# Kernel optimization log

Measured on AMD Instinct MI355X. Metric: run time of the kernel, lower is better.

The kernel has to match this reference:

```python
import jax, jax.numpy as jnp
import numpy as np

N_ATOMS = 100_000
N_EDGES = 6_400_000
N_MOL = 128
Z_MAX = 90
KE = 14.3996
CUTOFF = 5.0


def setup_inputs() -> dict:
    key = jax.random.key(0)
    ks = jax.random.split(key, 9)
    partial_charges = jax.random.normal(ks[0], (N_ATOMS,), dtype=jnp.float32)
    Z = jax.random.randint(ks[1], (N_ATOMS,), 0, Z_MAX, dtype=jnp.int32)
    # Born exponents typically ~6-12
    ns = jax.random.uniform(ks[2], (N_ATOMS,), dtype=jnp.float32) * 4.0 + 6.0
    idx_m = jnp.sort(jax.random.randint(ks[3], (N_ATOMS,), 0, N_MOL, dtype=jnp.int32))
    idx_m = idx_m.at[-1].set(N_MOL - 1)
    # displacement vectors with norms bounded away from 0 to keep 1/d^n finite in fp32
    dirs = jax.random.normal(ks[4], (N_EDGES, 3), dtype=jnp.float32)
    dirs = dirs / jnp.linalg.norm(dirs, axis=1, keepdims=True)
    lengths = jax.random.uniform(ks[5], (N_EDGES, 1), dtype=jnp.float32) * 4.5 + 1.0
    Rij = dirs * lengths
    idx_i = jax.random.randint(ks[6], (N_EDGES,), 0, N_ATOMS, dtype=jnp.int32)
    idx_j = jax.random.randint(ks[7], (N_EDGES,), 0, N_ATOMS, dtype=jnp.int32)
    is_film = jax.random.randint(ks[8], (N_ATOMS,), 0, 2, dtype=jnp.int32)
    # dense realization of r0_dict: keyed by (is_film_i, is_film_j, Z_i, Z_j)
    r0_table = jax.random.uniform(jax.random.fold_in(key, 99), (2, 2, Z_MAX, Z_MAX), dtype=jnp.float32) * 1.5 + 0.5
    return {
        "partial_charges": partial_charges, "Z": Z, "ns": ns, "idx_m": idx_m,
        "Rij": Rij, "idx_i": idx_i, "idx_j": idx_j, "is_film": is_film,
        "r0_table": r0_table,
    }


def reference(partial_charges, Z, ns, idx_m, Rij, idx_i, idx_j, is_film, r0_table):
    q = partial_charges
    q_ij = jnp.abs(q[idx_i] * q[idx_j])                      # [E]
    d_ij = jnp.linalg.norm(Rij, axis=1)                      # [E]
    n_ij = ns[idx_i] + ns[idx_j] / 2.0                       # [E]
    r0_ij = r0_table[is_film[idx_i], is_film[idx_j], Z[idx_i], Z[idx_j]]  # [E]
    B_ij = q_ij * r0_ij ** (n_ij - 1.0) / n_ij               # [E]
    # shifted Born potential: B * (1/d^n - 1/cutoff^n)
    potential = B_ij * (d_ij ** (-n_ij) - CUTOFF ** (-n_ij))
    potential = jnp.where(d_ij <= CUTOFF, potential, jnp.zeros_like(potential))
    y = jax.ops.segment_sum(potential, idx_i, num_segments=N_ATOMS)  # edge -> atom
    y = jax.ops.segment_sum(y, idx_m, num_segments=N_MOL)            # atom -> molecule
    return 0.5 * KE * y
```

## Files before the change

kernel.cpp:

```cpp
#include <hip/hip_runtime.h>

#define NMOL 128
#define ZMAX 90
#define BLOCK 256

__device__ __forceinline__ float fast_exp2(float x) {
#if __has_builtin(__builtin_amdgcn_exp2f)
    return __builtin_amdgcn_exp2f(x);
#else
    return exp2f(x);
#endif
}
__device__ __forceinline__ float fast_log2(float x) {
#if __has_builtin(__builtin_amdgcn_logf)
    return __builtin_amdgcn_logf(x);
#else
    return log2f(x);
#endif
}
__device__ __forceinline__ float fast_rcp(float x) {
#if __has_builtin(__builtin_amdgcn_rcpf)
    return __builtin_amdgcn_rcpf(x);
#else
    return 1.0f / x;
#endif
}

__global__ void pack_atoms_kernel(const float* __restrict__ q,
                                  const int* __restrict__ Z,
                                  const float* __restrict__ ns,
                                  const int* __restrict__ idx_m,
                                  const int* __restrict__ is_film,
                                  float4* __restrict__ atoms,
                                  float* __restrict__ out, int nA) {
    int t = blockIdx.x * BLOCK + threadIdx.x;
    if (blockIdx.x == 0 && threadIdx.x < NMOL) out[threadIdx.x] = 0.0f;
    if (t < nA) {
        float4 a;
        a.x = q[t];
        a.y = ns[t];
        a.z = __int_as_float(Z[t] | (is_film[t] << 16));
        a.w = __int_as_float(idx_m[t]);
        atoms[t] = a;
    }
}

__device__ __forceinline__ float edge_pot(const float4* __restrict__ atoms,
                                          const float* __restrict__ r0_table,
                                          int i, int j,
                                          float x, float y, float z,
                                          int& mol) {
    constexpr float LOG2_CUT = 2.321928094887362f;
    const float4 ai = atoms[i];
    const float4 aj = atoms[j];
    const float d2 = fmaf(x, x, fmaf(y, y, z * z));

    int zi = __float_as_int(ai.z);
    int zj = __float_as_int(aj.z);
    const int fi = zi >> 16, fj = zj >> 16;
    zi &= 0xFFFF; zj &= 0xFFFF;
    const float r0 = r0_table[((fi * 2 + fj) * ZMAX + zi) * ZMAX + zj];

    const float qij = fabsf(ai.x * aj.x);
    const float n = fmaf(0.5f, aj.y, ai.y);
    const float B = qij * fast_exp2((n - 1.0f) * fast_log2(r0)) * fast_rcp(n);
    const float dpow = fast_exp2(-0.5f * n * fast_log2(d2));
    const float cpow = fast_exp2(-n * LOG2_CUT);

    mol = __float_as_int(ai.w);
    return (d2 <= 25.0f) ? B * (dpow - cpow) : 0.0f;
}

__global__ void __launch_bounds__(BLOCK)
edge_kernel(const float4* __restrict__ atoms,
            const float* __restrict__ r0_table,
            const float4* __restrict__ Rij4,
            const int4* __restrict__ idx_i4,
            const int4* __restrict__ idx_j4,
            float* __restrict__ out, int nE) {
    constexpr float HALF_KE = 7.1998f;

    __shared__ float bins[NMOL];
    for (int t = threadIdx.x; t < NMOL; t += BLOCK) bins[t] = 0.0f;
    __syncthreads();

    const int nE4 = nE >> 2;
    const int stride = gridDim.x * BLOCK;
    for (int t = blockIdx.x * BLOCK + threadIdx.x; t < nE4; t += stride) {
        const int4 ii = idx_i4[t];
        const int4 jj = idx_j4[t];
        const float4 ra = Rij4[3 * t + 0];
        const float4 rb = Rij4[3 * t + 1];
        const float4 rc = Rij4[3 * t + 2];

        int m0, m1, m2, m3;
        const float p0 = edge_pot(atoms, r0_table, ii.x, jj.x, ra.x, ra.y, ra.z, m0);
        const float p1 = edge_pot(atoms, r0_table, ii.y, jj.y, ra.w, rb.x, rb.y, m1);
        const float p2 = edge_pot(atoms, r0_table, ii.z, jj.z, rb.z, rb.w, rc.x, m2);
        const float p3 = edge_pot(atoms, r0_table, ii.w, jj.w, rc.y, rc.z, rc.w, m3);

        if (p0 != 0.0f) atomicAdd(&bins[m0], p0);
        if (p1 != 0.0f) atomicAdd(&bins[m1], p1);
        if (p2 != 0.0f) atomicAdd(&bins[m2], p2);
        if (p3 != 0.0f) atomicAdd(&bins[m3], p3);
    }

    const int tail_start = nE4 << 2;
    const int* idx_i = (const int*)idx_i4;
    const int* idx_j = (const int*)idx_j4;
    const float* Rij = (const float*)Rij4;
    for (int e = tail_start + blockIdx.x * BLOCK + threadIdx.x; e < nE; e += stride) {
        int m;
        const float p = edge_pot(atoms, r0_table, idx_i[e], idx_j[e],
                                 Rij[3 * e + 0], Rij[3 * e + 1], Rij[3 * e + 2], m);
        if (p != 0.0f) atomicAdd(&bins[m], p);
    }

    __syncthreads();
    for (int t = threadIdx.x; t < NMOL; t += BLOCK) {
        const float v = bins[t];
        if (v != 0.0f) atomicAdd(&out[t], v * HALF_KE);
    }
}

__global__ void __launch_bounds__(BLOCK)
edge_kernel_raw(const float* __restrict__ q,
                const int* __restrict__ Z,
                const float* __restrict__ ns,
                const int* __restrict__ idx_m,
                const int* __restrict__ is_film,
                const float* __restrict__ r0_table,
                const float* __restrict__ Rij,
                const int* __restrict__ idx_i,
                const int* __restrict__ idx_j,
                float* __restrict__ out, int nE) {
    constexpr float HALF_KE = 7.1998f;
    constexpr float LOG2_CUT = 2.321928094887362f;

    __shared__ float bins[NMOL];
    for (int t = threadIdx.x; t < NMOL; t += BLOCK) bins[t] = 0.0f;
    __syncthreads();

    const int stride = gridDim.x * BLOCK;
    for (int e = blockIdx.x * BLOCK + threadIdx.x; e < nE; e += stride) {
        const int i = idx_i[e];
        const int j = idx_j[e];
        const float x = Rij[3 * e + 0];
        const float y = Rij[3 * e + 1];
        const float z = Rij[3 * e + 2];
        const float d2 = fmaf(x, x, fmaf(y, y, z * z));

        const float r0 = r0_table[((is_film[i] * 2 + is_film[j]) * ZMAX + Z[i]) * ZMAX + Z[j]];
        const float qij = fabsf(q[i] * q[j]);
        const float n = fmaf(0.5f, ns[j], ns[i]);
        const float B = qij * fast_exp2((n - 1.0f) * fast_log2(r0)) * fast_rcp(n);
        const float dpow = fast_exp2(-0.5f * n * fast_log2(d2));
        const float cpow = fast_exp2(-n * LOG2_CUT);

        if (d2 <= 25.0f) {
            atomicAdd(&bins[idx_m[i]], B * (dpow - cpow));
        }
    }

    __syncthreads();
    for (int t = threadIdx.x; t < NMOL; t += BLOCK) {
        const float v = bins[t];
        if (v != 0.0f) atomicAdd(&out[t], v * HALF_KE);
    }
}

__global__ void zero_out_kernel(float* __restrict__ out) {
    if (threadIdx.x < NMOL) out[threadIdx.x] = 0.0f;
}

extern "C" void kernel_launch(void* const* d_in, const int* in_sizes, int n_in,
                              void* d_out, int out_size, void* d_ws, size_t ws_size,
                              hipStream_t stream) {
    const float* q        = (const float*)d_in[0];
    const int*   Z        = (const int*)  d_in[1];
    const float* ns       = (const float*)d_in[2];
    const int*   idx_m    = (const int*)  d_in[3];
    const float* Rij      = (const float*)d_in[4];
    const int*   idx_i    = (const int*)  d_in[5];
    const int*   idx_j    = (const int*)  d_in[6];
    const int*   is_film  = (const int*)  d_in[7];
    const float* r0_table = (const float*)d_in[8];

    const int nA = in_sizes[0];
    const int nE = in_sizes[5];
    float* out = (float*)d_out;

    const size_t atoms_bytes = (size_t)nA * sizeof(float4);
    const int edge_grid = 2048;

    if (ws_size >= atoms_bytes) {
        float4* atoms = (float4*)d_ws;
        const int pack_grid = (nA + BLOCK - 1) / BLOCK;
        pack_atoms_kernel<<<pack_grid, BLOCK, 0, stream>>>(q, Z, ns, idx_m, is_film,
                                                           atoms, out, nA);
        edge_kernel<<<edge_grid, BLOCK, 0, stream>>>(atoms, r0_table,
                                                     (const float4*)Rij,
                                                     (const int4*)idx_i,
                                                     (const int4*)idx_j,
                                                     out, nE);
    } else {
        zero_out_kernel<<<1, BLOCK, 0, stream>>>(out);
        edge_kernel_raw<<<edge_grid, BLOCK, 0, stream>>>(q, Z, ns, idx_m, is_film, r0_table,
                                                         Rij, idx_i, idx_j, out, nE);
    }
}
```

Before: 234.9 us.

## Stage r0 table in LDS, use nontemporal streaming loads, resize edge grid

Each block of the edge kernel now copies the 16200-entry r0 table (about 64 KB) into shared memory and looks r0 up there instead of gathering it from global memory. Edge index and displacement streams are read with nontemporal loads so they do not push the atom table out of cache. All eight atom gathers are issued before any math to expose memory-level parallelism. The launch changes to 256 blocks of 1024 threads, which costs per-block table load time and uses a lot of LDS per block, limiting how many blocks fit per CU.

```diff
diff --git a/kernel.cpp b/kernel.cpp
--- a/kernel.cpp
+++ b/kernel.cpp
@@ -2,7 +2,13 @@
 
 #define NMOL 128
 #define ZMAX 90
-#define BLOCK 256
+#define TBL (2 * 2 * ZMAX * ZMAX)
+#define BLOCK_E 1024
+#define GRID_E 256
+#define BLOCK_P 256
+
+typedef float  fx4 __attribute__((ext_vector_type(4)));
+typedef int    ix4 __attribute__((ext_vector_type(4)));
 
 __device__ __forceinline__ float fast_exp2(float x) {
 #if __has_builtin(__builtin_amdgcn_exp2f)
@@ -33,7 +39,7 @@
                                   const int* __restrict__ is_film,
                                   float4* __restrict__ atoms,
                                   float* __restrict__ out, int nA) {
-    int t = blockIdx.x * BLOCK + threadIdx.x;
+    int t = blockIdx.x * BLOCK_P + threadIdx.x;
     if (blockIdx.x == 0 && threadIdx.x < NMOL) out[threadIdx.x] = 0.0f;
     if (t < nA) {
         float4 a;
@@ -45,85 +51,105 @@
     }
 }
 
-__device__ __forceinline__ float edge_pot(const float4* __restrict__ atoms,
-                                          const float* __restrict__ r0_table,
-                                          int i, int j,
-                                          float x, float y, float z,
-                                          int& mol) {
+__device__ __forceinline__ float pot_from(const float4& ai, const float4& aj,
+                                          float r0, float d2) {
     constexpr float LOG2_CUT = 2.321928094887362f;
-    const float4 ai = atoms[i];
-    const float4 aj = atoms[j];
-    const float d2 = fmaf(x, x, fmaf(y, y, z * z));
-
-    int zi = __float_as_int(ai.z);
-    int zj = __float_as_int(aj.z);
-    const int fi = zi >> 16, fj = zj >> 16;
-    zi &= 0xFFFF; zj &= 0xFFFF;
-    const float r0 = r0_table[((fi * 2 + fj) * ZMAX + zi) * ZMAX + zj];
-
     const float qij = fabsf(ai.x * aj.x);
     const float n = fmaf(0.5f, aj.y, ai.y);
     const float B = qij * fast_exp2((n - 1.0f) * fast_log2(r0)) * fast_rcp(n);
     const float dpow = fast_exp2(-0.5f * n * fast_log2(d2));
     const float cpow = fast_exp2(-n * LOG2_CUT);
-
-    mol = __float_as_int(ai.w);
     return (d2 <= 25.0f) ? B * (dpow - cpow) : 0.0f;
 }
 
-__global__ void __launch_bounds__(BLOCK)
+__device__ __forceinline__ int tbl_idx(const float4& ai, const float4& aj) {
+    int zi = __float_as_int(ai.z);
+    int zj = __float_as_int(aj.z);
+    const int fi = zi >> 16, fj = zj >> 16;
+    zi &= 0xFFFF; zj &= 0xFFFF;
+    return ((fi * 2 + fj) * ZMAX + zi) * ZMAX + zj;
+}
+
+__global__ void __launch_bounds__(BLOCK_E, 4)
 edge_kernel(const float4* __restrict__ atoms,
             const float* __restrict__ r0_table,
-            const float4* __restrict__ Rij4,
-            const int4* __restrict__ idx_i4,
-            const int4* __restrict__ idx_j4,
+            const fx4* __restrict__ Rij4,
+            const ix4* __restrict__ idx_i4,
+            const ix4* __restrict__ idx_j4,
             float* __restrict__ out, int nE) {
     constexpr float HALF_KE = 7.1998f;
 
+    __shared__ float r0_lds[TBL];
     __shared__ float bins[NMOL];
-    for (int t = threadIdx.x; t < NMOL; t += BLOCK) bins[t] = 0.0f;
+
+    {
+        const fx4* src = (const fx4*)r0_table;
+        fx4* dst = (fx4*)r0_lds;
+        for (int t = threadIdx.x; t < TBL / 4; t += BLOCK_E) dst[t] = src[t];
+    }
+    for (int t = threadIdx.x; t < NMOL; t += BLOCK_E) bins[t] = 0.0f;
     __syncthreads();
 
     const int nE4 = nE >> 2;
-    const int stride = gridDim.x * BLOCK;
-    for (int t = blockIdx.x * BLOCK + threadIdx.x; t < nE4; t += stride) {
-        const int4 ii = idx_i4[t];
-        const int4 jj = idx_j4[t];
-        const float4 ra = Rij4[3 * t + 0];
-        const float4 rb = Rij4[3 * t + 1];
-        const float4 rc = Rij4[3 * t + 2];
-
-        int m0, m1, m2, m3;
-        const float p0 = edge_pot(atoms, r0_table, ii.x, jj.x, ra.x, ra.y, ra.z, m0);
-        const float p1 = edge_pot(atoms, r0_table, ii.y, jj.y, ra.w, rb.x, rb.y, m1);
-        const float p2 = edge_pot(atoms, r0_table, ii.z, jj.z, rb.z, rb.w, rc.x, m2);
-        const float p3 = edge_pot(atoms, r0_table, ii.w, jj.w, rc.y, rc.z, rc.w, m3);
-
-        if (p0 != 0.0f) atomicAdd(&bins[m0], p0);
-        if (p1 != 0.0f) atomicAdd(&bins[m1], p1);
-        if (p2 != 0.0f) atomicAdd(&bins[m2], p2);
-        if (p3 != 0.0f) atomicAdd(&bins[m3], p3);
+    const int stride = gridDim.x * BLOCK_E;
+    for (int t = blockIdx.x * BLOCK_E + threadIdx.x; t < nE4; t += stride) {
+        const ix4 ii = __builtin_nontemporal_load(&idx_i4[t]);
+        const ix4 jj = __builtin_nontemporal_load(&idx_j4[t]);
+        const fx4 ra = __builtin_nontemporal_load(&Rij4[3 * t + 0]);
+        const fx4 rb = __builtin_nontemporal_load(&Rij4[3 * t + 1]);
+        const fx4 rc = __builtin_nontemporal_load(&Rij4[3 * t + 2]);
+
+        const float4 a0 = atoms[ii.x];
+        const float4 a1 = atoms[ii.y];
+        const float4 a2 = atoms[ii.z];
+        const float4 a3 = atoms[ii.w];
+        const float4 b0 = atoms[jj.x];
+        const float4 b1 = atoms[jj.y];
+        const float4 b2 = atoms[jj.z];
+        const float4 b3 = atoms[jj.w];
+
+        const float d20 = fmaf(ra.x, ra.x, fmaf(ra.y, ra.y, ra.z * ra.z));
+        const float d21 = fmaf(ra.w, ra.w, fmaf(rb.x, rb.x, rb.y * rb.y));
+        const float d22 = fmaf(rb.z, rb.z, fmaf(rb.w, rb.w, rc.x * rc.x));
+        const float d23 = fmaf(rc.y, rc.y, fmaf(rc.z, rc.z, rc.w * rc.w));
+
+        const float r00 = r0_lds[tbl_idx(a0, b0)];
+        const float r01 = r0_lds[tbl_idx(a1, b1)];
+        const float r02 = r0_lds[tbl_idx(a2, b2)];
+        const float r03 = r0_lds[tbl_idx(a3, b3)];
+
+        const float p0 = pot_from(a0, b0, r00, d20);
+        const float p1 = pot_from(a1, b1, r01, d21);
+        const float p2 = pot_from(a2, b2, r02, d22);
+        const float p3 = pot_from(a3, b3, r03, d23);
+
+        if (p0 != 0.0f) atomicAdd(&bins[__float_as_int(a0.w)], p0);
+        if (p1 != 0.0f) atomicAdd(&bins[__float_as_int(a1.w)], p1);
+        if (p2 != 0.0f) atomicAdd(&bins[__float_as_int(a2.w)], p2);
+        if (p3 != 0.0f) atomicAdd(&bins[__float_as_int(a3.w)], p3);
     }
 
     const int tail_start = nE4 << 2;
     const int* idx_i = (const int*)idx_i4;
     const int* idx_j = (const int*)idx_j4;
     const float* Rij = (const float*)Rij4;
-    for (int e = tail_start + blockIdx.x * BLOCK + threadIdx.x; e < nE; e += stride) {
-        int m;
-        const float p = edge_pot(atoms, r0_table, idx_i[e], idx_j[e],
-                                 Rij[3 * e + 0], Rij[3 * e + 1], Rij[3 * e + 2], m);
-        if (p != 0.0f) atomicAdd(&bins[m], p);
-    }
-
-    __syncthreads();
-    for (int t = threadIdx.x; t < NMOL; t += BLOCK) {
+    for (int e = tail_start + blockIdx.x * BLOCK_E + threadIdx.x; e < nE; e += stride) {
+        const float4 ai = atoms[idx_i[e]];
+        const float4 aj = atoms[idx_j[e]];
+        const float x = Rij[3 * e + 0], y = Rij[3 * e + 1], z = Rij[3 * e + 2];
+        const float d2 = fmaf(x, x, fmaf(y, y, z * z));
+        const float p = pot_from(ai, aj, r0_lds[tbl_idx(ai, aj)], d2);
+        if (p != 0.0f) atomicAdd(&bins[__float_as_int(ai.w)], p);
+    }
+
+    __syncthreads();
+    for (int t = threadIdx.x; t < NMOL; t += BLOCK_E) {
         const float v = bins[t];
         if (v != 0.0f) atomicAdd(&out[t], v * HALF_KE);
     }
 }
 
-__global__ void __launch_bounds__(BLOCK)
+__global__ void __launch_bounds__(BLOCK_P)
 edge_kernel_raw(const float* __restrict__ q,
                 const int* __restrict__ Z,
                 const float* __restrict__ ns,
@@ -138,32 +164,26 @@
     constexpr float LOG2_CUT = 2.321928094887362f;
 
     __shared__ float bins[NMOL];
-    for (int t = threadIdx.x; t < NMOL; t += BLOCK) bins[t] = 0.0f;
-    __syncthreads();
-
-    const int stride = gridDim.x * BLOCK;
-    for (int e = blockIdx.x * BLOCK + threadIdx.x; e < nE; e += stride) {
+    for (int t = threadIdx.x; t < NMOL; t += BLOCK_P) bins[t] = 0.0f;
+    __syncthreads();
+
+    const int stride = gridDim.x * BLOCK_P;
+    for (int e = blockIdx.x * BLOCK_P + threadIdx.x; e < nE; e += stride) {
         const int i = idx_i[e];
         const int j = idx_j[e];
-        const float x = Rij[3 * e + 0];
-        const float y = Rij[3 * e + 1];
-        const float z = Rij[3 * e + 2];
+        const float x = Rij[3 * e + 0], y = Rij[3 * e + 1], z = Rij[3 * e + 2];
         const float d2 = fmaf(x, x, fmaf(y, y, z * z));
-
         const float r0 = r0_table[((is_film[i] * 2 + is_film[j]) * ZMAX + Z[i]) * ZMAX + Z[j]];
         const float qij = fabsf(q[i] * q[j]);
         const float n = fmaf(0.5f, ns[j], ns[i]);
         const float B = qij * fast_exp2((n - 1.0f) * fast_log2(r0)) * fast_rcp(n);
         const float dpow = fast_exp2(-0.5f * n * fast_log2(d2));
         const float cpow = fast_exp2(-n * LOG2_CUT);
-
-        if (d2 <= 25.0f) {
-            atomicAdd(&bins[idx_m[i]], B * (dpow - cpow));
-        }
-    }
-
-    __syncthreads();
-    for (int t = threadIdx.x; t < NMOL; t += BLOCK) {
+        if (d2 <= 25.0f) atomicAdd(&bins[idx_m[i]], B * (dpow - cpow));
+    }
+
+    __syncthreads();
+    for (int t = threadIdx.x; t < NMOL; t += BLOCK_P) {
         const float v = bins[t];
         if (v != 0.0f) atomicAdd(&out[t], v * HALF_KE);
     }
@@ -191,21 +211,20 @@
     float* out = (float*)d_out;
 
     const size_t atoms_bytes = (size_t)nA * sizeof(float4);
-    const int edge_grid = 2048;
 
     if (ws_size >= atoms_bytes) {
         float4* atoms = (float4*)d_ws;
-        const int pack_grid = (nA + BLOCK - 1) / BLOCK;
-        pack_atoms_kernel<<<pack_grid, BLOCK, 0, stream>>>(q, Z, ns, idx_m, is_film,
-                                                           atoms, out, nA);
-        edge_kernel<<<edge_grid, BLOCK, 0, stream>>>(atoms, r0_table,
-                                                     (const float4*)Rij,
-                                                     (const int4*)idx_i,
-                                                     (const int4*)idx_j,
-                                                     out, nE);
+        const int pack_grid = (nA + BLOCK_P - 1) / BLOCK_P;
+        pack_atoms_kernel<<<pack_grid, BLOCK_P, 0, stream>>>(q, Z, ns, idx_m, is_film,
+                                                             atoms, out, nA);
+        edge_kernel<<<GRID_E, BLOCK_E, 0, stream>>>(atoms, r0_table,
+                                                    (const fx4*)Rij,
+                                                    (const ix4*)idx_i,
+                                                    (const ix4*)idx_j,
+                                                    out, nE);
     } else {
-        zero_out_kernel<<<1, BLOCK, 0, stream>>>(out);
-        edge_kernel_raw<<<edge_grid, BLOCK, 0, stream>>>(q, Z, ns, idx_m, is_film, r0_table,
-                                                         Rij, idx_i, idx_j, out, nE);
-    }
-}
+        zero_out_kernel<<<1, BLOCK_P, 0, stream>>>(out);
+        edge_kernel_raw<<<2048, BLOCK_P, 0, stream>>>(q, Z, ns, idx_m, is_film, r0_table,
+                                                      Rij, idx_i, idx_j, out, nE);
+    }
+}
```

New measurement: 236.9 us. Within noise of the previous version (+0.8%).
